# Optimization experiments

Hardware: AMD Instinct MI355X
Metric: run time of the kernel (lower is better)

The kernel has to match this reference:

```python
import jax, jax.numpy as jnp
from jax import lax
import numpy as np


def setup_inputs() -> dict:
    key = jax.random.key(0)
    kx, kw = jax.random.split(key)
    # Binary {0,1} activations: the module's int8-cast/XOR/AND trick is only
    # meaningful XNOR-popcount math for binary inputs.
    x = jax.random.randint(kx, (32, 256, 58, 58), 0, 2).astype(jnp.float32)
    weight = jax.random.normal(kw, (256, 256, 3, 3), dtype=jnp.float32)
    return {"x": x, "weight": weight}


def reference(x, weight):
    # XNORConv2d.forward, stride=1, padding=0 (forward never pads).
    B, C, H, W = x.shape
    O, _, kh, kw = weight.shape
    n = C * H * W  # note: alpha normalizes by INPUT size, as in the source
    N = kh * kw

    # alpha = sum_{c,kh,kw} |w| / n, one scalar per output filter  -> (O,)
    alpha = jnp.sum(jnp.abs(weight), axis=(1, 2, 3)) / n

    # Binarized weights: sign(w) >= 0 -> {0,1}
    bw = (weight >= 0).astype(x.dtype)

    dn = lax.conv_dimension_numbers(x.shape, weight.shape, ("NCHW", "OIHW", "NCHW"))
    conv = lambda a, f: lax.conv_general_dilated(
        a, f, window_strides=(1, 1), padding="VALID", dimension_numbers=dn
    )

    # XNOR match count per (b, o, y, x): S = #(p==f) over c,kh,kw
    #   = conv(p, f) + conv(1-p, 1-f)
    S = conv(x, bw) + conv(1.0 - x, 1.0 - bw)  # (B, O, H', W')

    # popcount per channel = 2*s_c - N; summed over channels -> 2*S - C*N
    res = 2.0 * S - jnp.asarray(C * N, dtype=x.dtype)

    return alpha[None, :, None, None] * res
```

## Files before the change

### kernel.cpp

```cpp
#include <hip/hip_runtime.h>
#include <stdint.h>


#define BATCH 32
#define C_IN 256
#define OCH 256
#define HIN 58
#define WIN2 58
#define HOUT 56
#define WOUT 56
#define TAPS 9
#define WWORDS 8
#define HWIN (HIN * WIN2)
#define HWOUT (HOUT * WOUT)
#define NPOS (BATCH * HWIN)

#define AP 144
#define NAPOS 232
#define BCH 8192

typedef int   i32x4  __attribute__((ext_vector_type(4)));
typedef int   i32x16 __attribute__((ext_vector_type(16)));
typedef float f32x4  __attribute__((ext_vector_type(4)));

#define MFMA(acc, va, vb) \
    asm volatile("v_mfma_i32_32x32x32_i8 %0, %1, %2, %0" : "+v"(acc) : "v"(va), "v"(vb))

__global__ __launch_bounds__(256) void pack_x_kernel(
    const float* __restrict__ x, uint32_t* __restrict__ xp)
{
    int t = blockIdx.x * 256 + threadIdx.x;
    int p  = t >> 2;
    int wp = t & 3;
    int b = p / HWIN;
    int r = p - b * HWIN;
    const float* xb = x + ((size_t)(b * C_IN + wp * 64)) * HWIN + r;
    uint32_t m0 = 0u, m1 = 0u;
    #pragma unroll
    for (int j = 0; j < 32; ++j) {
        float v0 = xb[(size_t)j * HWIN];
        float v1 = xb[(size_t)(j + 32) * HWIN];
        m0 |= (v0 > 0.5f ? 1u : 0u) << j;
        m1 |= (v1 > 0.5f ? 1u : 0u) << j;
    }
    *(uint2*)(xp + (size_t)p * WWORDS + wp * 2) = make_uint2(m0, m1);
}

__global__ __launch_bounds__(256) void pack_w8_kernel(
    const float* __restrict__ wt, char* __restrict__ wq8, float* __restrict__ sA)
{
    int o = blockIdx.x;
    int c = threadIdx.x;
    const float* wb = wt + ((size_t)o * C_IN + c) * TAPS;
    float s = 0.f;
    char sg[TAPS];
    #pragma unroll
    for (int t = 0; t < TAPS; ++t) {
        float v = wb[t];
        s += fabsf(v);
        sg[t] = (v >= 0.0f) ? (char)1 : (char)-1;
    }
    #pragma unroll
    for (int t = 0; t < TAPS; ++t)
        wq8[(size_t)o * (TAPS * C_IN) + t * C_IN + c] = sg[t];

    __shared__ float red[256];
    red[c] = s;
    __syncthreads();
    for (int off = 128; off > 0; off >>= 1) {
        if (c < off) red[c] += red[c + off];
        __syncthreads();
    }
    if (c == 0) sA[o] = red[0] / (float)(C_IN * HWIN);
}

__global__ __launch_bounds__(512)
__attribute__((amdgpu_waves_per_eu(4, 4)))
void xnor_mfma_kernel(
    const uint32_t* __restrict__ xp, const char* __restrict__ wq8,
    const float* __restrict__ sA, float* __restrict__ out)
{
    __shared__ __attribute__((aligned(16))) char lds[NAPOS * AP + 2 * BCH];
    char* Alds = lds;
    char* Blds = lds + NAPOS * AP;
    float* Cbuf = (float*)lds;

    int blk = blockIdx.x;
    int b   = blk / 28;
    int rp  = blk - b * 28;
    int oy0 = rp * 2;
    int tid  = threadIdx.x;
    int wv   = tid >> 6;
    int lane = tid & 63;
    int l31  = lane & 31;
    int e    = lane >> 5;
    int mgrp = wv & 1;
    int ngrp = wv >> 1;

    int baseA[2];
    #pragma unroll
    for (int mi = 0; mi < 2; ++mi) {
        int p = (mgrp * 2 + mi) * 32 + l31;
        int r = (p * 586) >> 15;
        int c = p - 56 * r;
        baseA[mi] = (r * 58 + c) * AP + e * 16;
    }
    int bofsB = (ngrp * 64 + l31) * 32 + e * 16;
    float al0 = sA[ngrp * 64 + l31];
    float al1 = sA[ngrp * 64 + 32 + l31];

    i32x16 acc00 = {0}, acc01 = {0}, acc10 = {0}, acc11 = {0};
    asm volatile("" : "+v"(acc00), "+v"(acc01), "+v"(acc10), "+v"(acc11));
    asm volatile("s_nop 7\n\ts_nop 7");

#define STAGE_A(KH)                                                        \
    {                                                                      \
        _Pragma("unroll")                                                  \
        for (int ir = 0; ir < 4; ++ir) {                                   \
            if (tid < 464) {                                               \
                int iw = tid >> 3, c16 = tid & 7;                          \
                uint32_t wvx = xp[((size_t)(b * HIN + oy0 + ir) * WIN2 + iw) * WWORDS \
                                  + (KH) * 4 + (c16 >> 1)];                \
                uint32_t bits = (c16 & 1) ? (wvx >> 16) : (wvx & 0xFFFFu); \
                i32x4 v;                                                   \
                _Pragma("unroll")                                          \
                for (int d = 0; d < 4; ++d) {                              \
                    uint32_t n  = (bits >> (4 * d)) & 0xFu;                \
                    uint32_t sp = (n * 0x204081u) & 0x01010101u;           \
                    v[d] = (int)~(sp * 0xFEu);                             \
                }                                                          \
                *(i32x4*)(Alds + (ir * 58 + iw) * AP + c16 * 16) = v;      \
            }                                                              \
        }                                                                  \
    }

    STAGE_A(0);

    const char* wqt = wq8 + (size_t)(tid >> 1) * (TAPS * C_IN) + (tid & 1) * 16;
    char* bw = Blds + ((tid >> 1) * 32 + (tid & 1) * 16);
    i32x4 regP = *(const i32x4*)(wqt + 0);
    *(i32x4*)(bw + 0) = regP;
    regP = *(const i32x4*)(wqt + 32);
    __syncthreads();

    #pragma unroll
    for (int s = 0; s < 72; ++s) {
        if (s == 36) { STAGE_A(1); __syncthreads(); }
        const int kh  = s / 36;
        const int tap = (s - kh * 36) >> 2;
        const int kb  = s & 3;
        const int dy  = tap / 3, dx = tap - dy * 3;
        const int s2   = (s + 2 > 71) ? 71 : s + 2;
        const int kh2  = s2 / 36;
        const int tap2 = (s2 - kh2 * 36) >> 2;
        const int kb2  = s2 & 3;
        i32x4 regN = *(const i32x4*)(wqt + tap2 * 256 + kh2 * 128 + kb2 * 32);

        const int ka = (dy * 58 + dx) * AP + kb * 32;
        const char* Br = Blds + (s & 1) * BCH;
        i32x4 a0 = *(const i32x4*)(Alds + baseA[0] + ka);
        i32x4 a1 = *(const i32x4*)(Alds + baseA[1] + ka);
        i32x4 b0 = *(const i32x4*)(Br + bofsB);
        i32x4 b1 = *(const i32x4*)(Br + bofsB + 1024);
        MFMA(acc00, a0, b0);
        MFMA(acc01, a0, b1);
        MFMA(acc10, a1, b0);
        MFMA(acc11, a1, b1);

        *(i32x4*)(bw + ((s & 1) ^ 1) * BCH) = regP;
        regP = regN;
        __syncthreads();
    }

    asm volatile("s_nop 7\n\ts_nop 7");

    size_t ob = ((size_t)b * OCH) * HWOUT + (size_t)oy0 * WOUT;
    #pragma unroll
    for (int q = 0; q < 4; ++q) {
        __syncthreads();
        if (mgrp == (q >> 1)) {
            const int mi = q & 1;
            #pragma unroll
            for (int ni = 0; ni < 2; ++ni) {
                float al = ni ? al1 : al0;
                int o = ngrp * 64 + ni * 32 + l31;
                i32x16 A;
                if (mi == 0 && ni == 0) A = acc00;
                else if (mi == 0)       A = acc01;
                else if (ni == 0)       A = acc10;
                else                    A = acc11;
                #pragma unroll
                for (int g = 0; g < 4; ++g) {
                    f32x4 vv;
                    vv[0] = al * (float)A[4 * g + 0];
                    vv[1] = al * (float)A[4 * g + 1];
                    vv[2] = al * (float)A[4 * g + 2];
                    vv[3] = al * (float)A[4 * g + 3];
                    int pl = g * 8 + 4 * e;
                    *(f32x4*)(Cbuf + (size_t)o * 36 + pl) = vv;
                }
            }
        }
        __syncthreads();
        #pragma unroll 1
        for (int i = 0; i < 16; ++i) {
            int idx = i * 512 + tid;
            int o = idx >> 5, pl = idx & 31;
            int pg = q * 32 + pl;
            if (pg < 112) {
                int r = (pg >= 56) ? 1 : 0;
                int c = pg - 56 * r;
                out[ob + (size_t)o * HWOUT + r * WOUT + c] = Cbuf[o * 36 + pl];
            }
        }
    }
#undef STAGE_A
}

extern "C" void kernel_launch(void* const* d_in, const int* in_sizes, int n_in,
                              void* d_out, int out_size, void* d_ws, size_t ws_size,
                              hipStream_t stream)
{
    const float* x  = (const float*)d_in[0];
    const float* wt = (const float*)d_in[1];
    float* out = (float*)d_out;

    char* ws = (char*)d_ws;
    uint32_t* xp  = (uint32_t*)ws;
    char*     wq8 = (char*)(ws + 3444736);
    float*    sAp = (float*)(ws + 3444736 + 589824);

    pack_x_kernel<<<dim3(1682), dim3(256), 0, stream>>>(x, xp);

    pack_w8_kernel<<<dim3(OCH), dim3(256), 0, stream>>>(wt, wq8, sAp);

    xnor_mfma_kernel<<<dim3(896), dim3(512), 0, stream>>>(xp, wq8, sAp, out);
}
```

Before: 285.3 us.

## Load MFMA B operands directly from global into registers, drop LDS double buffer

Weights are pre-swizzled by the packing kernel into a per-step, per-lane layout, so each lane loads its MFMA B fragments straight from global/L2 into a 3-deep register ring. This removes the per-step LDS store and the __syncthreads in the 72-step main loop, and shrinks LDS use. The fixed waves-per-EU attribute is also removed. In exchange, each wave issues its own global loads, which now carry redundant traffic across waves that share the same output channels, and global latency must be hidden by only three steps of prefetch.

```diff
diff --git a/kernel.cpp b/kernel.cpp
--- a/kernel.cpp
+++ b/kernel.cpp
@@ -17,7 +17,6 @@
 
 #define AP 144
 #define NAPOS 232
-#define BCH 8192
 
 typedef int   i32x4  __attribute__((ext_vector_type(4)));
 typedef int   i32x16 __attribute__((ext_vector_type(16)));
@@ -47,7 +46,7 @@
 }
 
 __global__ __launch_bounds__(256) void pack_w8_kernel(
-    const float* __restrict__ wt, char* __restrict__ wq8, float* __restrict__ sA)
+    const float* __restrict__ wt, char* __restrict__ wq8s, float* __restrict__ sA)
 {
     int o = blockIdx.x;
     int c = threadIdx.x;
@@ -60,9 +59,15 @@
         s += fabsf(v);
         sg[t] = (v >= 0.0f) ? (char)1 : (char)-1;
     }
-    #pragma unroll
-    for (int t = 0; t < TAPS; ++t)
-        wq8[(size_t)o * (TAPS * C_IN) + t * C_IN + c] = sg[t];
+    int kh = c >> 7;
+    int kb = (c >> 5) & 3;
+    int e  = (c >> 4) & 1;
+    int j  = c & 15;
+    #pragma unroll
+    for (int t = 0; t < TAPS; ++t) {
+        int st = kh * 36 + t * 4 + kb;
+        wq8s[(size_t)((st * 2 + e) * 256 + o) * 16 + j] = sg[t];
+    }
 
     __shared__ float red[256];
     red[c] = s;
@@ -75,14 +80,12 @@
 }
 
 __global__ __launch_bounds__(512)
-__attribute__((amdgpu_waves_per_eu(4, 4)))
 void xnor_mfma_kernel(
-    const uint32_t* __restrict__ xp, const char* __restrict__ wq8,
+    const uint32_t* __restrict__ xp, const char* __restrict__ wq8s,
     const float* __restrict__ sA, float* __restrict__ out)
 {
-    __shared__ __attribute__((aligned(16))) char lds[NAPOS * AP + 2 * BCH];
+    __shared__ __attribute__((aligned(16))) char lds[36864];
     char* Alds = lds;
-    char* Blds = lds + NAPOS * AP;
     float* Cbuf = (float*)lds;
 
     int blk = blockIdx.x;
@@ -105,7 +108,7 @@
         int c = p - 56 * r;
         baseA[mi] = (r * 58 + c) * AP + e * 16;
     }
-    int bofsB = (ngrp * 64 + l31) * 32 + e * 16;
+    const char* pb = wq8s + ((size_t)e * 256 + (size_t)(ngrp * 64 + l31)) * 16;
     float al0 = sA[ngrp * 64 + l31];
     float al1 = sA[ngrp * 64 + 32 + l31];
 
@@ -136,40 +139,39 @@
 
     STAGE_A(0);
 
-    const char* wqt = wq8 + (size_t)(tid >> 1) * (TAPS * C_IN) + (tid & 1) * 16;
-    char* bw = Blds + ((tid >> 1) * 32 + (tid & 1) * 16);
-    i32x4 regP = *(const i32x4*)(wqt + 0);
-    *(i32x4*)(bw + 0) = regP;
-    regP = *(const i32x4*)(wqt + 32);
+    i32x4 rb0[3], rb1[3];
+    #pragma unroll
+    for (int q = 0; q < 3; ++q) {
+        rb0[q] = *(const i32x4*)(pb + (size_t)q * 8192);
+        rb1[q] = *(const i32x4*)(pb + (size_t)q * 8192 + 512);
+    }
     __syncthreads();
 
     #pragma unroll
     for (int s = 0; s < 72; ++s) {
-        if (s == 36) { STAGE_A(1); __syncthreads(); }
+        if (s == 36) {
+            __syncthreads();
+            STAGE_A(1);
+            __syncthreads();
+        }
         const int kh  = s / 36;
         const int tap = (s - kh * 36) >> 2;
         const int kb  = s & 3;
         const int dy  = tap / 3, dx = tap - dy * 3;
-        const int s2   = (s + 2 > 71) ? 71 : s + 2;
-        const int kh2  = s2 / 36;
-        const int tap2 = (s2 - kh2 * 36) >> 2;
-        const int kb2  = s2 & 3;
-        i32x4 regN = *(const i32x4*)(wqt + tap2 * 256 + kh2 * 128 + kb2 * 32);
-
-        const int ka = (dy * 58 + dx) * AP + kb * 32;
-        const char* Br = Blds + (s & 1) * BCH;
+        const int ka  = (dy * 58 + dx) * AP + kb * 32;
+
         i32x4 a0 = *(const i32x4*)(Alds + baseA[0] + ka);
         i32x4 a1 = *(const i32x4*)(Alds + baseA[1] + ka);
-        i32x4 b0 = *(const i32x4*)(Br + bofsB);
-        i32x4 b1 = *(const i32x4*)(Br + bofsB + 1024);
+        i32x4 b0 = rb0[s % 3];
+        i32x4 b1 = rb1[s % 3];
         MFMA(acc00, a0, b0);
         MFMA(acc01, a0, b1);
         MFMA(acc10, a1, b0);
         MFMA(acc11, a1, b1);
 
-        *(i32x4*)(bw + ((s & 1) ^ 1) * BCH) = regP;
-        regP = regN;
-        __syncthreads();
+        const int s3 = (s + 3 > 71) ? 71 : s + 3;
+        rb0[s % 3] = *(const i32x4*)(pb + (size_t)s3 * 8192);
+        rb1[s % 3] = *(const i32x4*)(pb + (size_t)s3 * 8192 + 512);
     }
 
     asm volatile("s_nop 7\n\ts_nop 7");
@@ -226,13 +228,13 @@
     float* out = (float*)d_out;
 
     char* ws = (char*)d_ws;
-    uint32_t* xp  = (uint32_t*)ws;
-    char*     wq8 = (char*)(ws + 3444736);
-    float*    sAp = (float*)(ws + 3444736 + 589824);
+    uint32_t* xp   = (uint32_t*)ws;
+    char*     wq8s = (char*)(ws + 3444736);
+    float*    sAp  = (float*)(ws + 3444736 + 589824);
 
     pack_x_kernel<<<dim3(1682), dim3(256), 0, stream>>>(x, xp);
 
-    pack_w8_kernel<<<dim3(OCH), dim3(256), 0, stream>>>(wt, wq8, sAp);
-
-    xnor_mfma_kernel<<<dim3(896), dim3(512), 0, stream>>>(xp, wq8, sAp, out);
-}
+    pack_w8_kernel<<<dim3(OCH), dim3(256), 0, stream>>>(wt, wq8s, sAp);
+
+    xnor_mfma_kernel<<<dim3(896), dim3(512), 0, stream>>>(xp, wq8s, sAp, out);
+}
```

Result: faster. 268.9 us (-5.8%).
